# Kernel tuning notes

Hardware: AMD Instinct MI355X
Metric: run time of the kernel (lower is better)

Reference implementation:

```python
import jax, jax.numpy as jnp
import numpy as np
from jax import lax

EPS = 1e-5

# --- ApproxSign (ReActNet binary activation, STE with polynomial grad) ---
@jax.custom_vjp
def approx_sign(x):
    return jnp.sign(x)

def _as_fwd(x):
    return jnp.sign(x), x

def _as_bwd(x, g):
    # d/dx of piecewise-polynomial approx: 2-2|x| for |x|<1, else 0
    return (g * jnp.maximum(0.0, 2.0 - 2.0 * jnp.abs(x)),)

approx_sign.defvjp(_as_fwd, _as_bwd)


def rsign(x, bias):
    # learnable per-channel shift then binarize
    return approx_sign(x + bias[None, :, None, None])


def scaled_sign_weight(w):
    # per-output-channel scale * sign(w); straight-through identity grad to w
    scale = jnp.mean(jnp.abs(w), axis=(1, 2, 3), keepdims=True)
    bw = scale * jnp.sign(w)
    return lax.stop_gradient(bw - w) + w


def conv(x, w, stride, pad):
    return lax.conv_general_dilated(
        x, w, window_strides=(stride, stride), padding=[(pad, pad), (pad, pad)],
        dimension_numbers=("NCHW", "OIHW", "NCHW"))


def bn(x, g, b, m, v):
    inv = g / jnp.sqrt(v + EPS)
    return x * inv[None, :, None, None] + (b - m * inv)[None, :, None, None]


def rprelu(x, gamma, beta, zeta):
    t = x - gamma[None, :, None, None]
    return jnp.where(t > 0, t, beta[None, :, None, None] * t) + zeta[None, :, None, None]


def avgpool2(x):
    B, C, H, W = x.shape
    return x.reshape(B, C, H // 2, 2, W // 2, 2).mean(axis=(3, 5))


def setup_inputs() -> dict:
    key = jax.random.key(0)
    ks = jax.random.split(key, 16)
    C = 256
    d = {}
    d["x"] = jax.random.normal(ks[0], (64, C, 28, 28), dtype=jnp.float32)
    d["rsign_bias"] = jax.random.normal(ks[1], (C,), dtype=jnp.float32) * 0.1
    d["w1"] = jax.random.normal(ks[2], (C, C, 3, 3), dtype=jnp.float32) * 0.05
    d["bn1_g"] = jnp.ones((C,), jnp.float32)
    d["bn1_b"] = jnp.zeros((C,), jnp.float32)
    d["bn1_m"] = jax.random.normal(ks[3], (C,), dtype=jnp.float32) * 0.1
    d["bn1_v"] = jax.random.uniform(ks[4], (C,), dtype=jnp.float32, minval=0.5, maxval=1.5)
    d["w21"] = jax.random.normal(ks[5], (C, C, 1, 1), dtype=jnp.float32) * 0.05
    d["bn21_g"] = jnp.ones((C,), jnp.float32)
    d["bn21_b"] = jnp.zeros((C,), jnp.float32)
    d["bn21_m"] = jax.random.normal(ks[6], (C,), dtype=jnp.float32) * 0.1
    d["bn21_v"] = jax.random.uniform(ks[7], (C,), dtype=jnp.float32, minval=0.5, maxval=1.5)
    d["w22"] = jax.random.normal(ks[8], (C, C, 1, 1), dtype=jnp.float32) * 0.05
    d["bn22_g"] = jnp.ones((C,), jnp.float32)
    d["bn22_b"] = jnp.zeros((C,), jnp.float32)
    d["bn22_m"] = jax.random.normal(ks[9], (C,), dtype=jnp.float32) * 0.1
    d["bn22_v"] = jax.random.uniform(ks[10], (C,), dtype=jnp.float32, minval=0.5, maxval=1.5)
    d["pr_gamma"] = jax.random.normal(ks[11], (C,), dtype=jnp.float32) * 0.1
    d["pr_beta"] = jnp.full((C,), 0.25, jnp.float32)
    d["pr_zeta"] = jax.random.normal(ks[12], (C,), dtype=jnp.float32) * 0.1
    return d


def reference(x, rsign_bias, w1, bn1_g, bn1_b, bn1_m, bn1_v,
              w21, bn21_g, bn21_b, bn21_m, bn21_v,
              w22, bn22_g, bn22_b, bn22_m, bn22_v,
              pr_gamma, pr_beta, pr_zeta):
    # layer1: RSign -> 3x3 stride2 binary conv -> BN
    out = bn(conv(rsign(x, rsign_bias), scaled_sign_weight(w1), 2, 1),
             bn1_g, bn1_b, bn1_m, bn1_v)
    out1 = out + avgpool2(x)                       # residual with avgpooled input
    out2 = rprelu(out1, pr_gamma, pr_beta, pr_zeta)
    # two parallel 1x1 binary conv branches (shared RSign bias)
    a = rsign(out2, rsign_bias)
    out2_1 = bn(conv(a, scaled_sign_weight(w21), 1, 0), bn21_g, bn21_b, bn21_m, bn21_v)
    out2_2 = bn(conv(a, scaled_sign_weight(w22), 1, 0), bn22_g, bn22_b, bn22_m, bn22_v)
    out4_1 = rprelu(out2_1 + out2, pr_gamma, pr_beta, pr_zeta)
    out4_2 = rprelu(out2_2 + out2, pr_gamma, pr_beta, pr_zeta)
    return jnp.concatenate([out4_1, out4_2], axis=1)  # [B, 2C, H/2, W/2]
```

## Files before the change

kernel.cpp:

```cpp
#include <hip/hip_runtime.h>
#include <stdint.h>

#define EPS_BN 1e-5f

#define C 256
#define H 28
#define W 28
#define R196 196
#define M_TOT 12544
#define K1 2304

typedef __attribute__((ext_vector_type(4))) int   i32x4;
typedef __attribute__((ext_vector_type(4))) float f32x4;
typedef unsigned short ushort_t;
typedef unsigned int uint_t;

__device__ __forceinline__ char sgn_i8(float v) {
    return v > 0.f ? (char)1 : (v < 0.f ? (char)-1 : (char)0);
}
__device__ __forceinline__ uint_t sgn_b(float v) {
    return (uint_t)(unsigned char)sgn_i8(v);
}

__device__ __forceinline__ void gload16(const void* g, void* l) {
    __builtin_amdgcn_global_load_lds(
        (const __attribute__((address_space(1))) void*)g,
        (__attribute__((address_space(3))) void*)l, 16, 0, 0);
}


__global__ __launch_bounds__(256) void prep_sign(
    const float* __restrict__ w1,
    const float* __restrict__ bn1_g, const float* __restrict__ bn1_b,
    const float* __restrict__ bn1_m, const float* __restrict__ bn1_v,
    const float* __restrict__ w21,
    const float* __restrict__ bn21_g, const float* __restrict__ bn21_b,
    const float* __restrict__ bn21_m, const float* __restrict__ bn21_v,
    const float* __restrict__ w22,
    const float* __restrict__ bn22_g, const float* __restrict__ bn22_b,
    const float* __restrict__ bn22_m, const float* __restrict__ bn22_v,
    const float* __restrict__ x, const float* __restrict__ bias,
    char* __restrict__ bw1, char* __restrict__ bw2,
    float* __restrict__ alpha1, float* __restrict__ beta1,
    float* __restrict__ alpha2, float* __restrict__ beta2,
    char* __restrict__ a1p, float* __restrict__ pool)
{
    __shared__ uint_t lsign[1792];
    float* red = (float*)lsign;
    const int bid = blockIdx.x;
    const int t = threadIdx.x;

    if (bid < 768) {
        if (bid < 256) {
            const int oc = bid;
            const float* w = w1 + oc * K1;
            float s = 0.f;
            for (int i = t; i < K1; i += 256) s += fabsf(w[i]);
            red[t] = s; __syncthreads();
            for (int o = 128; o > 0; o >>= 1) {
                if (t < o) red[t] += red[t + o];
                __syncthreads();
            }
            const float scale = red[0] * (1.f / (float)K1);
            if (t == 0) {
                const float inv = bn1_g[oc] * rsqrtf(bn1_v[oc] + EPS_BN);
                alpha1[oc] = scale * inv;
                beta1[oc]  = bn1_b[oc] - bn1_m[oc] * inv;
            }
            const int ic = ((t & 3) << 6) | (t >> 2);
#pragma unroll
            for (int tap = 0; tap < 9; ++tap)
                bw1[oc * K1 + tap * 256 + t] = sgn_i8(w[ic * 9 + tap]);
        } else {
            const bool br2 = (bid >= 512);
            const int oc = (bid - 256) & 255;
            const float* w = (br2 ? w22 : w21) + oc * 256;
            red[t] = fabsf(w[t]); __syncthreads();
            for (int o = 128; o > 0; o >>= 1) {
                if (t < o) red[t] += red[t + o];
                __syncthreads();
            }
            const float scale = red[0] * (1.f / 256.f);
            const int n = oc + (br2 ? 256 : 0);
            if (t == 0) {
                const float g = br2 ? bn22_g[oc] : bn21_g[oc];
                const float b = br2 ? bn22_b[oc] : bn21_b[oc];
                const float m = br2 ? bn22_m[oc] : bn21_m[oc];
                const float v = br2 ? bn22_v[oc] : bn22_v[oc];
                const float v2 = br2 ? bn22_v[oc] : bn21_v[oc];
                (void)v;
                const float inv = g * rsqrtf(v2 + EPS_BN);
                alpha2[n] = scale * inv;
                beta2[n]  = b - m * inv;
            }
            bw2[n * 256 + t] = sgn_i8(w[t]);
        }
        return;
    }

    const int sb = bid - 768;
    const int hh = sb & 1;
    const int bo = sb >> 1;
    const int b = bo / 14, oh = bo % 14;
    const float* xb = x + (size_t)(b * 256) * 784 + (2 * oh) * 28;

    for (int i = t; i < 896; i += 256) {
        const int lc = i / 7, q = i - lc * 7;
        const int c = 64 * (lc >> 5) + 32 * hh + (lc & 31);
        const float bc = bias[c];
        const float4 v0 = *(const float4*)(xb + c * 784 + 4 * q);
        const float4 v1 = *(const float4*)(xb + c * 784 + 28 + 4 * q);
        uint_t s0 = sgn_b(v0.x + bc) | (sgn_b(v0.y + bc) << 8) |
                    (sgn_b(v0.z + bc) << 16) | (sgn_b(v0.w + bc) << 24);
        uint_t s1 = sgn_b(v1.x + bc) | (sgn_b(v1.y + bc) << 8) |
                    (sgn_b(v1.z + bc) << 16) | (sgn_b(v1.w + bc) << 24);
        lsign[lc * 7 + q] = s0;
        lsign[896 + lc * 7 + q] = s1;
        float2 pr;
        pr.x = 0.25f * (v0.x + v0.y + v1.x + v1.y);
        pr.y = 0.25f * (v0.z + v0.w + v1.z + v1.w);
        *(float2*)(pool + (size_t)(b * 256 + c) * 196 + oh * 14 + 2 * q) = pr;
    }
    __syncthreads();

    for (int i = t; i < 448; i += 256) {
        const int tl = i & 31;
        const int q = (i >> 5) % 7;
        const int row = i / 224;
        const int tt = 32 * hh + tl;
        uint_t d[4];
#pragma unroll
        for (int e = 0; e < 4; ++e)
            d[e] = lsign[row * 896 + (tl + 32 * e) * 7 + q];
        char* orow = a1p + (size_t)((b * 30 + 2 * oh + row + 1) * 30) * 256;
#pragma unroll
        for (int j = 0; j < 4; ++j) {
            uint_t o = ((d[0] >> (8 * j)) & 0xffu)
                     | (((d[1] >> (8 * j)) & 0xffu) << 8)
                     | (((d[2] >> (8 * j)) & 0xffu) << 16)
                     | (((d[3] >> (8 * j)) & 0xffu) << 24);
            *(uint_t*)(orow + (4 * q + j + 1) * 256 + 4 * tt) = o;
        }
    }

    {
        char* orow0 = a1p + (size_t)((b * 30 + 2 * oh + 1) * 30) * 256;
        char* orow1 = a1p + (size_t)((b * 30 + 2 * oh + 2) * 30) * 256;
        const int bo2 = 128 * hh + (t & 127);
        if (t < 128) { orow0[bo2] = 0; orow1[bo2] = 0; }
        else         { orow0[29 * 256 + bo2] = 0; orow1[29 * 256 + bo2] = 0; }
    }
    if (oh == 0) {
        char* r0  = a1p + (size_t)(b * 900) * 256;
        char* r29 = a1p + (size_t)(b * 900 + 29 * 30) * 256;
        for (int idx = t; idx < 30 * 128; idx += 256) {
            const int colo = (idx >> 7) * 256 + 128 * hh + (idx & 127);
            r0[colo] = 0; r29[colo] = 0;
        }
    }
}

__global__ __launch_bounds__(512) void conv1_i8(
    const char* __restrict__ a1p,
    const char* __restrict__ bw1,
    const float* __restrict__ alpha1, const float* __restrict__ beta1,
    const float* __restrict__ p,
    const float* __restrict__ rsb,
    const float* __restrict__ prg, const float* __restrict__ prb,
    const float* __restrict__ prz,
    float* __restrict__ out2,
    char* __restrict__ a2)
{
    __shared__ char lA[2][64 * 128];
    __shared__ char lB[2][64 * 128];

    const int bid = blockIdx.x;
    const int wgid = (bid & 7) * 98 + (bid >> 3);
    const int mtile = wgid >> 2;
    const int ntile = wgid & 3;

    const int tid = threadIdx.x;
    const int wave = tid >> 6;
    const int lane = tid & 63;
    const int col = lane & 15;
    const int krow = lane >> 4;
    const int wr = wave >> 2;
    const int wc = wave & 3;
    const int l8 = lane >> 3;
    const int s8 = lane & 7;
    const int swz = ((s8 ^ l8) << 4);

    int pbA;
    {
        const int grow = wave * 8 + l8;
        const int m = mtile * 64 + grow;
        const int b = m / 196, r = m % 196;
        const int oh = r / 14, ow = r % 14;
        pbA = ((b * 30 + 2 * oh) * 30 + 2 * ow) * 256 + swz;
    }
    const int pbB = (ntile * 64 + wave * 8 + l8) * K1 + swz;

    int rswz[2];
#pragma unroll
    for (int ks = 0; ks < 2; ++ks)
        rswz[ks] = ((ks * 4 + krow) ^ (col & 7)) << 4;

    const int n0e = ntile * 64 + wc * 16 + krow * 4;
    float p_pre[2][4];
#pragma unroll
    for (int im = 0; im < 2; ++im) {
        const int m = mtile * 64 + wr * 32 + im * 16 + col;
        const int b = m / 196, r = m % 196;
#pragma unroll
        for (int j = 0; j < 4; ++j)
            p_pre[im][j] = p[(b * 256 + n0e + j) * 196 + r];
    }

    i32x4 acc[2] = {};

    auto stage = [&](int step, int buf) {
        const int tap = step >> 1;
        const int kc0 = (step & 1) << 7;
        const int kh = tap / 3, kw = tap - kh * 3;
        const int aoff = (kh * 30 + kw) * 256 + kc0;
        gload16(a1p + pbA + aoff, &lA[buf][0] + wave * 1024);
        gload16(bw1 + pbB + step * 128, &lB[buf][0] + wave * 1024);
    };

    stage(0, 0);

    int cur = 0;
    for (int step = 0; step < 18; ++step) {
        if (step + 1 < 18) {
            stage(step + 1, cur ^ 1);
            asm volatile("s_waitcnt vmcnt(2)" ::: "memory");
        } else {
            asm volatile("s_waitcnt vmcnt(0)" ::: "memory");
        }
        __builtin_amdgcn_s_barrier();
        __builtin_amdgcn_sched_barrier(0);

#pragma unroll
        for (int ks = 0; ks < 2; ++ks) {
            i32x4 bf[2], af;
#pragma unroll
            for (int im = 0; im < 2; ++im) {
                const int row = wr * 32 + im * 16 + col;
                bf[im] = *(const i32x4*)(&lA[cur][0] + row * 128 + rswz[ks]);
            }
            {
                const int row = wc * 16 + col;
                af = *(const i32x4*)(&lB[cur][0] + row * 128 + rswz[ks]);
            }
#pragma unroll
            for (int im = 0; im < 2; ++im)
                acc[im] = __builtin_amdgcn_mfma_i32_16x16x64_i8(
                    af, bf[im], acc[im], 0, 0, 0);
        }
        __builtin_amdgcn_sched_barrier(0);
        __builtin_amdgcn_s_barrier();
        cur ^= 1;
    }

    float* otile = (float*)&lA[0][0];
    char*  atile = &lB[0][0];
    __syncthreads();
#pragma unroll
    for (int im = 0; im < 2; ++im) {
        const int ml = wr * 32 + im * 16 + col;
#pragma unroll
        for (int j = 0; j < 4; ++j) {
            const int nl = wc * 16 + krow * 4 + j;
            const int n = ntile * 64 + nl;
            float v = alpha1[n] * (float)acc[im][j] + beta1[n] + p_pre[im][j];
            const float t = v - prg[n];
            const float o = (t > 0.f ? t : prb[n] * t) + prz[n];
            otile[nl * 64 + ml] = o;
            atile[ml * 64 + nl] = sgn_i8(o + rsb[n]);
        }
    }
    __syncthreads();
    {
        const int m = mtile * 64 + lane;
        const int b = m / 196, r = m % 196;
#pragma unroll
        for (int nn = 0; nn < 8; ++nn) {
            const int nl = wave * 8 + nn;
            out2[(b * 256 + ntile * 64 + nl) * 196 + r] = otile[nl * 64 + lane];
        }
    }
    {
        const uint_t* at32 = (const uint_t*)atile;
#pragma unroll
        for (int h = 0; h < 2; ++h) {
            const int idx = h * 512 + tid;
            const int ml = idx >> 4, nq = idx & 15;
            *(uint_t*)(a2 + (size_t)(mtile * 64 + ml) * 256 + ntile * 64 + nq * 4)
                = at32[ml * 16 + nq];
        }
    }
}

__global__ __launch_bounds__(512) void conv1x1_i8(
    const char* __restrict__ a2,
    const char* __restrict__ bw2,
    const float* __restrict__ alpha2, const float* __restrict__ beta2,
    const float* __restrict__ out2,
    const float* __restrict__ prg, const float* __restrict__ prb,
    const float* __restrict__ prz,
    float* __restrict__ out)
{
    __shared__ char lA[2][64 * 128];
    __shared__ char lB[2][64 * 128];

    const int bid = blockIdx.x;
    const int wgid = (bid & 7) * 196 + (bid >> 3);
    const int mtile = wgid >> 3;
    const int ntile = wgid & 7;

    const int tid = threadIdx.x;
    const int wave = tid >> 6;
    const int lane = tid & 63;
    const int col = lane & 15;
    const int krow = lane >> 4;
    const int wr = wave >> 2;
    const int wc = wave & 3;
    const int l8 = lane >> 3;
    const int s8 = lane & 7;
    const int swz = ((s8 ^ l8) << 4);

    const int pbA = (mtile * 64 + wave * 8 + l8) * 256 + swz;
    const int pbB = (ntile * 64 + wave * 8 + l8) * 256 + swz;

    const int n0e = ntile * 64 + wc * 16 + krow * 4;
    float o2_pre[2][4];
#pragma unroll
    for (int im = 0; im < 2; ++im) {
        const int m = mtile * 64 + wr * 32 + im * 16 + col;
        const int b = m / 196, r = m % 196;
#pragma unroll
        for (int j = 0; j < 4; ++j)
            o2_pre[im][j] = out2[(b * 256 + ((n0e + j) & 255)) * 196 + r];
    }

#pragma unroll
    for (int h = 0; h < 2; ++h) {
        gload16(a2 + pbA + h * 128, &lA[h][0] + wave * 1024);
        gload16(bw2 + pbB + h * 128, &lB[h][0] + wave * 1024);
    }
    asm volatile("s_waitcnt vmcnt(0)" ::: "memory");
    __builtin_amdgcn_s_barrier();
    __builtin_amdgcn_sched_barrier(0);

    i32x4 acc[2] = {};
#pragma unroll
    for (int ks = 0; ks < 4; ++ks) {
        const int h = ks >> 1, k2 = ks & 1;
        const int ro = ((k2 * 4 + krow) ^ (col & 7)) << 4;
        i32x4 bf[2], af;
#pragma unroll
        for (int im = 0; im < 2; ++im) {
            const int row = wr * 32 + im * 16 + col;
            bf[im] = *(const i32x4*)(&lA[h][0] + row * 128 + ro);
        }
        {
            const int row = wc * 16 + col;
            af = *(const i32x4*)(&lB[h][0] + row * 128 + ro);
        }
#pragma unroll
        for (int im = 0; im < 2; ++im)
            acc[im] = __builtin_amdgcn_mfma_i32_16x16x64_i8(
                af, bf[im], acc[im], 0, 0, 0);
    }

    float* otile = (float*)&lA[0][0];
    __syncthreads();
#pragma unroll
    for (int im = 0; im < 2; ++im) {
        const int ml = wr * 32 + im * 16 + col;
#pragma unroll
        for (int j = 0; j < 4; ++j) {
            const int nl = wc * 16 + krow * 4 + j;
            const int n = ntile * 64 + nl;
            const int oc = n & 255;
            float v = alpha2[n] * (float)acc[im][j] + beta2[n] + o2_pre[im][j];
            const float t = v - prg[oc];
            otile[nl * 64 + ml] = (t > 0.f ? t : prb[oc] * t) + prz[oc];
        }
    }
    __syncthreads();
    {
        const int m = mtile * 64 + lane;
        const int b = m / 196, r = m % 196;
#pragma unroll
        for (int nn = 0; nn < 8; ++nn) {
            const int nl = wave * 8 + nn;
            out[(size_t)(b * 512 + ntile * 64 + nl) * 196 + r]
                = otile[nl * 64 + lane];
        }
    }
}

extern "C" void kernel_launch(void* const* d_in, const int* in_sizes, int n_in,
                              void* d_out, int out_size, void* d_ws, size_t ws_size,
                              hipStream_t stream)
{
    (void)in_sizes; (void)n_in; (void)out_size; (void)ws_size;

    const float* x         = (const float*)d_in[0];
    const float* rsign_b   = (const float*)d_in[1];
    const float* w1        = (const float*)d_in[2];
    const float* bn1_g     = (const float*)d_in[3];
    const float* bn1_b     = (const float*)d_in[4];
    const float* bn1_m     = (const float*)d_in[5];
    const float* bn1_v     = (const float*)d_in[6];
    const float* w21       = (const float*)d_in[7];
    const float* bn21_g    = (const float*)d_in[8];
    const float* bn21_b    = (const float*)d_in[9];
    const float* bn21_m    = (const float*)d_in[10];
    const float* bn21_v    = (const float*)d_in[11];
    const float* w22       = (const float*)d_in[12];
    const float* bn22_g    = (const float*)d_in[13];
    const float* bn22_b    = (const float*)d_in[14];
    const float* bn22_m    = (const float*)d_in[15];
    const float* bn22_v    = (const float*)d_in[16];
    const float* pr_gamma  = (const float*)d_in[17];
    const float* pr_beta   = (const float*)d_in[18];
    const float* pr_zeta   = (const float*)d_in[19];

    char* ws = (char*)d_ws;
    size_t off = 0;
    char* a1p     = (char*)(ws + off);  off += (size_t)14745600;
    char* bw1     = (char*)(ws + off);  off += (size_t)589824;
    char* bw2     = (char*)(ws + off);  off += (size_t)131072;
    float* pool   = (float*)(ws + off); off += (size_t)3211264 * 4;
    float* out2   = (float*)(ws + off); off += (size_t)3211264 * 4;
    char* a2      = (char*)(ws + off);  off += (size_t)3211264;
    float* alpha1 = (float*)(ws + off); off += 1024;
    float* beta1  = (float*)(ws + off); off += 1024;
    float* alpha2 = (float*)(ws + off); off += 2048;
    float* beta2  = (float*)(ws + off); off += 2048;

    prep_sign<<<2560, 256, 0, stream>>>(
        w1, bn1_g, bn1_b, bn1_m, bn1_v,
        w21, bn21_g, bn21_b, bn21_m, bn21_v,
        w22, bn22_g, bn22_b, bn22_m, bn22_v,
        x, rsign_b,
        bw1, bw2, alpha1, beta1, alpha2, beta2, a1p, pool);

    conv1_i8<<<784, 512, 0, stream>>>(
        a1p, bw1, alpha1, beta1, pool, rsign_b,
        pr_gamma, pr_beta, pr_zeta, out2, a2);

    conv1x1_i8<<<1568, 512, 0, stream>>>(
        a2, bw2, alpha2, beta2, out2,
        pr_gamma, pr_beta, pr_zeta, (float*)d_out);
}
```

Baseline: 58.10 us.

## Retile prep_sign input packing to half-image by 64-channel blocks with coalesced stores

Each prep_sign activation block now handles 64 channels over half an image (14 input rows) instead of two input rows across half the channels. This halves the block count and packs the signs through a padded LDS layout. Padded-border zeroing is folded into the same blocks. The w1 sign repacking now reads nine contiguous weights per thread, fixing the tap/channel ordering, which changes the bw1 layout that conv1 consumes. The intent is fewer blocks and better-coalesced global reads and writes when building the padded int8 activation tensor, at the cost of more LDS per block and fewer blocks to spread across the GPU.

Result: faster. 53.89 us (-7.3%).

```diff
diff --git a/kernel.cpp b/kernel.cpp
--- a/kernel.cpp
+++ b/kernel.cpp
@@ -45,7 +45,7 @@
     float* __restrict__ alpha2, float* __restrict__ beta2,
     char* __restrict__ a1p, float* __restrict__ pool)
 {
-    __shared__ uint_t lsign[1792];
+    __shared__ uint_t lsign[64 * 99];
     float* red = (float*)lsign;
     const int bid = blockIdx.x;
     const int t = threadIdx.x;
@@ -54,8 +54,12 @@
         if (bid < 256) {
             const int oc = bid;
             const float* w = w1 + oc * K1;
+            float wv[9];
+#pragma unroll
+            for (int k = 0; k < 9; ++k) wv[k] = w[t * 9 + k];
             float s = 0.f;
-            for (int i = t; i < K1; i += 256) s += fabsf(w[i]);
+#pragma unroll
+            for (int k = 0; k < 9; ++k) s += fabsf(wv[k]);
             red[t] = s; __syncthreads();
             for (int o = 128; o > 0; o >>= 1) {
                 if (t < o) red[t] += red[t + o];
@@ -67,10 +71,9 @@
                 alpha1[oc] = scale * inv;
                 beta1[oc]  = bn1_b[oc] - bn1_m[oc] * inv;
             }
-            const int ic = ((t & 3) << 6) | (t >> 2);
 #pragma unroll
             for (int tap = 0; tap < 9; ++tap)
-                bw1[oc * K1 + tap * 256 + t] = sgn_i8(w[ic * 9 + tap]);
+                bw1[oc * K1 + tap * 256 + t] = sgn_i8(wv[tap]);
         } else {
             const bool br2 = (bid >= 512);
             const int oc = (bid - 256) & 255;
@@ -86,10 +89,8 @@
                 const float g = br2 ? bn22_g[oc] : bn21_g[oc];
                 const float b = br2 ? bn22_b[oc] : bn21_b[oc];
                 const float m = br2 ? bn22_m[oc] : bn21_m[oc];
-                const float v = br2 ? bn22_v[oc] : bn22_v[oc];
-                const float v2 = br2 ? bn22_v[oc] : bn21_v[oc];
-                (void)v;
-                const float inv = g * rsqrtf(v2 + EPS_BN);
+                const float v = br2 ? bn22_v[oc] : bn21_v[oc];
+                const float inv = g * rsqrtf(v + EPS_BN);
                 alpha2[n] = scale * inv;
                 beta2[n]  = b - m * inv;
             }
@@ -99,63 +100,58 @@
     }
 
     const int sb = bid - 768;
-    const int hh = sb & 1;
-    const int bo = sb >> 1;
-    const int b = bo / 14, oh = bo % 14;
-    const float* xb = x + (size_t)(b * 256) * 784 + (2 * oh) * 28;
-
-    for (int i = t; i < 896; i += 256) {
-        const int lc = i / 7, q = i - lc * 7;
-        const int c = 64 * (lc >> 5) + 32 * hh + (lc & 31);
+    const int rh = sb & 1;
+    const int cq = (sb >> 1) & 3;
+    const int b = sb >> 3;
+    const float* xb = x + ((size_t)(b * 256 + 64 * cq) * 784 + rh * 392);
+
+    for (int i = t; i < 3136; i += 256) {
+        const int cc = i / 49, o = i - cc * 49;
+        const int ihp = o / 7, q = o - ihp * 7;
+        const int c = 64 * cq + cc;
         const float bc = bias[c];
-        const float4 v0 = *(const float4*)(xb + c * 784 + 4 * q);
-        const float4 v1 = *(const float4*)(xb + c * 784 + 28 + 4 * q);
-        uint_t s0 = sgn_b(v0.x + bc) | (sgn_b(v0.y + bc) << 8) |
-                    (sgn_b(v0.z + bc) << 16) | (sgn_b(v0.w + bc) << 24);
-        uint_t s1 = sgn_b(v1.x + bc) | (sgn_b(v1.y + bc) << 8) |
-                    (sgn_b(v1.z + bc) << 16) | (sgn_b(v1.w + bc) << 24);
-        lsign[lc * 7 + q] = s0;
-        lsign[896 + lc * 7 + q] = s1;
+        const float* src = xb + cc * 784 + (2 * ihp) * 28 + 4 * q;
+        const float4 v0 = *(const float4*)src;
+        const float4 v1 = *(const float4*)(src + 28);
+        lsign[cc * 99 + (2 * ihp) * 7 + q] =
+            sgn_b(v0.x + bc) | (sgn_b(v0.y + bc) << 8) |
+            (sgn_b(v0.z + bc) << 16) | (sgn_b(v0.w + bc) << 24);
+        lsign[cc * 99 + (2 * ihp + 1) * 7 + q] =
+            sgn_b(v1.x + bc) | (sgn_b(v1.y + bc) << 8) |
+            (sgn_b(v1.z + bc) << 16) | (sgn_b(v1.w + bc) << 24);
         float2 pr;
         pr.x = 0.25f * (v0.x + v0.y + v1.x + v1.y);
         pr.y = 0.25f * (v0.z + v0.w + v1.z + v1.w);
-        *(float2*)(pool + (size_t)(b * 256 + c) * 196 + oh * 14 + 2 * q) = pr;
+        *(float2*)(pool + (size_t)(b * 256 + c) * 196
+                   + (7 * rh + ihp) * 14 + 2 * q) = pr;
     }
     __syncthreads();
 
-    for (int i = t; i < 448; i += 256) {
-        const int tl = i & 31;
-        const int q = (i >> 5) % 7;
-        const int row = i / 224;
-        const int tt = 32 * hh + tl;
-        uint_t d[4];
-#pragma unroll
-        for (int e = 0; e < 4; ++e)
-            d[e] = lsign[row * 896 + (tl + 32 * e) * 7 + q];
-        char* orow = a1p + (size_t)((b * 30 + 2 * oh + row + 1) * 30) * 256;
-#pragma unroll
-        for (int j = 0; j < 4; ++j) {
-            uint_t o = ((d[0] >> (8 * j)) & 0xffu)
-                     | (((d[1] >> (8 * j)) & 0xffu) << 8)
-                     | (((d[2] >> (8 * j)) & 0xffu) << 16)
-                     | (((d[3] >> (8 * j)) & 0xffu) << 24);
-            *(uint_t*)(orow + (4 * q + j + 1) * 256 + 4 * tt) = o;
-        }
-    }
-
     {
-        char* orow0 = a1p + (size_t)((b * 30 + 2 * oh + 1) * 30) * 256;
-        char* orow1 = a1p + (size_t)((b * 30 + 2 * oh + 2) * 30) * 256;
-        const int bo2 = 128 * hh + (t & 127);
-        if (t < 128) { orow0[bo2] = 0; orow1[bo2] = 0; }
-        else         { orow0[29 * 256 + bo2] = 0; orow1[29 * 256 + bo2] = 0; }
-    }
-    if (oh == 0) {
-        char* r0  = a1p + (size_t)(b * 900) * 256;
-        char* r29 = a1p + (size_t)(b * 900 + 29 * 30) * 256;
-        for (int idx = t; idx < 30 * 128; idx += 256) {
-            const int colo = (idx >> 7) * 256 + 128 * hh + (idx & 127);
-            r0[colo] = 0; r29[colo] = 0;
+        const int tw = t & 15;
+        for (int ii = (t >> 4); ii < 392; ii += 16) {
+            const int row = ii / 28, qj = ii - row * 28;
+            const int q = qj >> 2, j = qj & 3;
+            uint_t d[4];
+#pragma unroll
+            for (int e = 0; e < 4; ++e)
+                d[e] = lsign[(4 * tw + e) * 99 + row * 7 + q];
+            const uint_t ov = ((d[0] >> (8 * j)) & 0xffu)
+                            | (((d[1] >> (8 * j)) & 0xffu) << 8)
+                            | (((d[2] >> (8 * j)) & 0xffu) << 16)
+                            | (((d[3] >> (8 * j)) & 0xffu) << 24);
+            const int ihp = 14 * rh + row + 1;
+            const int iwp = 4 * q + j + 1;
+            *(uint_t*)(a1p + (size_t)((b * 30 + ihp) * 30 + iwp) * 256
+                       + 64 * cq + 4 * tw) = ov;
+        }
+        for (int px = (t >> 4); px < 60; px += 16) {
+            int ihp, iwp;
+            if (px < 15)      { ihp = 15 * rh + px;        iwp = 0;  }
+            else if (px < 30) { ihp = 15 * rh + (px - 15); iwp = 29; }
+            else              { ihp = 29 * rh;             iwp = px - 30; }
+            *(uint_t*)(a1p + (size_t)((b * 30 + ihp) * 30 + iwp) * 256
+                       + 64 * cq + 4 * tw) = 0u;
         }
     }
 }
@@ -441,7 +437,7 @@
     float* alpha2 = (float*)(ws + off); off += 2048;
     float* beta2  = (float*)(ws + off); off += 2048;
 
-    prep_sign<<<2560, 256, 0, stream>>>(
+    prep_sign<<<1280, 256, 0, stream>>>(
         w1, bn1_g, bn1_b, bn1_m, bn1_v,
         w21, bn21_g, bn21_b, bn21_m, bn21_v,
         w22, bn22_g, bn22_b, bn22_m, bn22_v,
```
